# Optimization experiments

Measured on AMD Instinct MI355X. Metric: run time of the kernel, lower is better.

## Reference

```python
import jax, jax.numpy as jnp
import numpy as np

N = 80000
E = 1280000
IN_DIM = 512
OUT_DIM = 64
POS_DIM = 8
NEG_SLOPE = 0.01  # F.leaky_relu default


def setup_inputs() -> dict:
    key = jax.random.key(0)
    k1, k2, k3, k4, k5, k6 = jax.random.split(key, 6)
    h = jax.random.normal(k1, (N, IN_DIM), dtype=jnp.float32)
    pos = jax.random.normal(k2, (N, POS_DIM), dtype=jnp.float32)
    src = jax.random.randint(k3, (E,), 0, N, dtype=jnp.int32)
    dst = jax.random.randint(k4, (E,), 0, N, dtype=jnp.int32)
    W_fc = jax.random.normal(k5, (OUT_DIM, IN_DIM), dtype=jnp.float32) * (1.0 / np.sqrt(IN_DIM))
    W_attn = jax.random.normal(k6, (1, 2 * OUT_DIM + 2 * POS_DIM), dtype=jnp.float32) * 0.1
    return {"h": h, "pos": pos, "src": src, "dst": dst, "W_fc": W_fc, "W_attn": W_attn}


def reference(h, pos, src, dst, W_fc, W_attn):
    # node projection: z = fc(h)  [N, out]
    z = h @ W_fc.T
    # attn_fc applied to concat([z_src, z_dst, pos_src, pos_dst]) == split dot products
    wa = W_attn[0]
    w_zs = wa[:OUT_DIM]
    w_zd = wa[OUT_DIM:2 * OUT_DIM]
    w_ps = wa[2 * OUT_DIM:2 * OUT_DIM + POS_DIM]
    w_pd = wa[2 * OUT_DIM + POS_DIM:]
    el = z @ w_zs + pos @ w_ps  # [N] src-side score
    er = z @ w_zd + pos @ w_pd  # [N] dst-side score
    e = el[src] + er[dst]       # [E]
    e = jnp.where(e > 0, e, NEG_SLOPE * e)  # leaky_relu
    # segment softmax over incoming edges of each dst node (numerically stable)
    emax = jax.ops.segment_max(e, dst, num_segments=N)  # [N]
    ex = jnp.exp(e - emax[dst])                         # [E]
    denom = jax.ops.segment_sum(ex, dst, num_segments=N)  # [N]
    alpha = ex / denom[dst]                             # [E]
    # weighted scatter-sum of src features
    msgs = alpha[:, None] * z[src]                      # [E, out]
    h_out = jax.ops.segment_sum(msgs, dst, num_segments=N)  # [N, out]
    return h_out
```

## Files before the change

kernel.cpp:

```cpp
#include <hip/hip_runtime.h>
#include <math.h>

#define N_NODES 80000
#define E_EDGES 1280000
#define IN_DIM  512
#define OUT_DIM 64
#define POS_DIM 8
#define NEG_SLOPE 0.01f

#define NB_BUCKET 313
#define BCAP 8192
#define SCAT_CHUNK 4096
#define SCAT_NB 313
#define GEMM_NB 625

#define BM 128
#define BK 64
#define LDA 72
#define LDB 72

typedef __attribute__((ext_vector_type(8))) short short8v;
typedef __attribute__((ext_vector_type(4))) float f32x4;

__device__ __forceinline__ unsigned short f2bf(float f) {
    unsigned u = __float_as_uint(f);
    unsigned r = u + 0x7fff + ((u >> 16) & 1);
    return (unsigned short)(r >> 16);
}
__device__ __forceinline__ float lrelu(float e) { return e > 0.f ? e : NEG_SLOPE * e; }

__global__ __launch_bounds__(256) void gemm_scatter(const float* __restrict__ h,
                                                    const float* __restrict__ W,
                                                    const float* __restrict__ pos,
                                                    const float* __restrict__ Wa,
                                                    const int* __restrict__ src,
                                                    const int* __restrict__ dst,
                                                    char* __restrict__ zq,
                                                    float* __restrict__ scl,
                                                    float* __restrict__ el,
                                                    float* __restrict__ er,
                                                    int* __restrict__ bcnt,
                                                    int* __restrict__ ebuf) {
    __shared__ unsigned short sA[BM][LDA];
    __shared__ unsigned short sB[64][LDB];
    __shared__ int hh[NB_BUCKET];
    __shared__ int gb[NB_BUCKET];
    const int t = threadIdx.x;

    if (blockIdx.x >= GEMM_NB) {
        const int e0 = (blockIdx.x - GEMM_NB) * SCAT_CHUNK;
        for (int i = t; i < NB_BUCKET; i += 256) hh[i] = 0;
        __syncthreads();

        int key[16];
        short bk[16];
        short lr[16];
        #pragma unroll
        for (int r = 0; r < 16; ++r) {
            const int e = e0 + r * 256 + t;
            if (e < E_EDGES) {
                const int d = dst[e];
                const int s = src[e];
                bk[r]  = (short)(d >> 8);
                key[r] = (s << 8) | (d & 255);
                lr[r]  = (short)atomicAdd(&hh[d >> 8], 1);
            } else {
                bk[r] = -1;
            }
        }
        __syncthreads();

        for (int i = t; i < NB_BUCKET; i += 256) {
            const int c = hh[i];
            gb[i] = c ? (i * BCAP + atomicAdd(&bcnt[i], c)) : 0;
        }
        __syncthreads();

        #pragma unroll
        for (int r = 0; r < 16; ++r) {
            if (bk[r] >= 0) {
                ebuf[gb[bk[r]] + lr[r]] = key[r];
            }
        }
        return;
    }

    const int lane = t & 63;
    const int w    = t >> 6;
    const int row0 = blockIdx.x * BM;
    const int g    = lane >> 4;
    const int rr   = lane & 15;

    f32x4 acc[2][4] = {};
    float4 ra[8];
    float4 rb[4];

    {
        #pragma unroll
        for (int i = 0; i < 8; ++i) {
            const int idx = t + i * 256;
            ra[i] = *(const float4*)&h[(size_t)(row0 + (idx >> 4)) * IN_DIM + ((idx & 15) << 2)];
        }
        #pragma unroll
        for (int i = 0; i < 4; ++i) {
            const int idx = t + i * 256;
            rb[i] = *(const float4*)&W[(size_t)(idx >> 4) * IN_DIM + ((idx & 15) << 2)];
        }
    }

    for (int c = 0; c < IN_DIM / BK; ++c) {
        __syncthreads();
        #pragma unroll
        for (int i = 0; i < 8; ++i) {
            const int idx = t + i * 256;
            ushort4 v = {f2bf(ra[i].x), f2bf(ra[i].y), f2bf(ra[i].z), f2bf(ra[i].w)};
            *(ushort4*)&sA[idx >> 4][(idx & 15) << 2] = v;
        }
        #pragma unroll
        for (int i = 0; i < 4; ++i) {
            const int idx = t + i * 256;
            ushort4 v = {f2bf(rb[i].x), f2bf(rb[i].y), f2bf(rb[i].z), f2bf(rb[i].w)};
            *(ushort4*)&sB[idx >> 4][(idx & 15) << 2] = v;
        }
        __syncthreads();

        if (c < IN_DIM / BK - 1) {
            const int k0 = (c + 1) * BK;
            #pragma unroll
            for (int i = 0; i < 8; ++i) {
                const int idx = t + i * 256;
                ra[i] = *(const float4*)&h[(size_t)(row0 + (idx >> 4)) * IN_DIM + k0 + ((idx & 15) << 2)];
            }
            #pragma unroll
            for (int i = 0; i < 4; ++i) {
                const int idx = t + i * 256;
                rb[i] = *(const float4*)&W[(size_t)(idx >> 4) * IN_DIM + k0 + ((idx & 15) << 2)];
            }
        }

        short8v afr[2][2];
        #pragma unroll
        for (int rt = 0; rt < 2; ++rt)
            #pragma unroll
            for (int ks = 0; ks < 2; ++ks)
                afr[rt][ks] = *(const short8v*)&sA[w * 32 + rt * 16 + rr][ks * 32 + g * 8];
        short8v bfr[4][2];
        #pragma unroll
        for (int ct = 0; ct < 4; ++ct)
            #pragma unroll
            for (int ks = 0; ks < 2; ++ks)
                bfr[ct][ks] = *(const short8v*)&sB[ct * 16 + rr][ks * 32 + g * 8];

        #pragma unroll
        for (int ks = 0; ks < 2; ++ks)
            #pragma unroll
            for (int rt = 0; rt < 2; ++rt)
                #pragma unroll
                for (int ct = 0; ct < 4; ++ct)
                    acc[rt][ct] = __builtin_amdgcn_mfma_f32_16x16x32_bf16(
                        afr[rt][ks], bfr[ct][ks], acc[rt][ct], 0, 0, 0);
    }

    __syncthreads();
    char* sI8 = (char*)sB;

    float wzs_c[4], wzd_c[4];
    #pragma unroll
    for (int ct = 0; ct < 4; ++ct) {
        wzs_c[ct] = Wa[ct * 16 + rr];
        wzd_c[ct] = Wa[OUT_DIM + ct * 16 + rr];
    }
    #pragma unroll
    for (int rt = 0; rt < 2; ++rt)
        #pragma unroll
        for (int r = 0; r < 4; ++r) {
            float pe = 0.f, pd = 0.f, rmax = 0.f;
            #pragma unroll
            for (int ct = 0; ct < 4; ++ct) {
                const float v = acc[rt][ct][r];
                pe += v * wzs_c[ct];
                pd += v * wzd_c[ct];
                rmax = fmaxf(rmax, fabsf(v));
            }
            #pragma unroll
            for (int off = 8; off; off >>= 1) {
                pe += __shfl_xor(pe, off);
                pd += __shfl_xor(pd, off);
                rmax = fmaxf(rmax, __shfl_xor(rmax, off));
            }
            rmax = fmaxf(rmax, 1e-20f);
            const float inv_s = 127.f / rmax;
            const int rloc = w * 32 + rt * 16 + g * 4 + r;
            #pragma unroll
            for (int ct = 0; ct < 4; ++ct) {
                int q = __float2int_rn(acc[rt][ct][r] * inv_s);
                q = max(-127, min(127, q));
                sI8[rloc * 64 + ct * 16 + rr] = (char)q;
            }
            if (rr == 0) {
                const int row = row0 + rloc;
                scl[row] = rmax * (1.f / 127.f);
                const float4 p0 = *(const float4*)&pos[(size_t)row * POS_DIM];
                const float4 p1 = *(const float4*)&pos[(size_t)row * POS_DIM + 4];
                const float4 s0 = *(const float4*)&Wa[2 * OUT_DIM];
                const float4 s1 = *(const float4*)&Wa[2 * OUT_DIM + 4];
                const float4 d0 = *(const float4*)&Wa[2 * OUT_DIM + POS_DIM];
                const float4 d1 = *(const float4*)&Wa[2 * OUT_DIM + POS_DIM + 4];
                el[row] = pe + p0.x * s0.x + p0.y * s0.y + p0.z * s0.z + p0.w * s0.w
                              + p1.x * s1.x + p1.y * s1.y + p1.z * s1.z + p1.w * s1.w;
                er[row] = pd + p0.x * d0.x + p0.y * d0.y + p0.z * d0.z + p0.w * d0.w
                              + p1.x * d1.x + p1.y * d1.y + p1.z * d1.z + p1.w * d1.w;
            }
        }

    __syncthreads();
    uint4* g4 = (uint4*)(zq + (size_t)row0 * 64);
    const uint4* s4 = (const uint4*)sI8;
    g4[t] = s4[t];
    g4[t + 256] = s4[t + 256];
}

__global__ __launch_bounds__(256) void bucket_csr(int* __restrict__ ebuf,
                                                  const int* __restrict__ bcnt,
                                                  int* __restrict__ offs,
                                                  int* __restrict__ oend) {
    __shared__ int se[BCAP];
    __shared__ int cnt[256];
    __shared__ int cur[256];
    __shared__ int wt[4];
    const int b = blockIdx.x;
    const int t = threadIdx.x;
    const int lane = t & 63;
    const int w = t >> 6;
    const int lo = b * BCAP;
    const int ne = min(bcnt[b], BCAP);

    cnt[t] = 0;
    __syncthreads();

    for (int i = t; i < ne; i += 256) {
        const int k = ebuf[lo + i];
        atomicAdd(&cnt[k & 255], 1);
        se[i] = k;
    }
    __syncthreads();

    const int v = cnt[t];
    int s = v;
    #pragma unroll
    for (int off = 1; off < 64; off <<= 1) {
        const int u = __shfl_up(s, off);
        if (lane >= off) s += u;
    }
    if (lane == 63) wt[w] = s;
    __syncthreads();
    int base = 0;
    #pragma unroll
    for (int i = 0; i < 4; ++i)
        if (i < w) base += wt[i];
    const int excl = base + s - v;
    cur[t] = excl;
    const int node = b * 256 + t;
    if (node < N_NODES) {
        offs[node] = lo + excl;
        oend[node] = lo + excl + v;
    }
    __syncthreads();

    for (int i = t; i < ne; i += 256) {
        const int k = se[i];
        const int p = atomicAdd(&cur[k & 255], 1);
        ebuf[lo + p] = k >> 8;
    }
}

__global__ __launch_bounds__(256) void aggregate(const int* __restrict__ offs,
                                                 const int* __restrict__ oend,
                                                 const int* __restrict__ esrc,
                                                 const float* __restrict__ el,
                                                 const float* __restrict__ er,
                                                 const float* __restrict__ scl,
                                                 const char* __restrict__ zq,
                                                 float* __restrict__ out) {
    const int widx = (int)((blockIdx.x * 256 + threadIdx.x) >> 6);
    const int lane = threadIdx.x & 63;
    const int g = lane >> 4;
    const int u = lane & 15;
    const int d = widx * 4 + g;
    if (d >= N_NODES) return;
    const int start = offs[d];
    const int ne    = oend[d] - start;
    const float erd = er[d];
    const int bl = g << 4;

    int sA = 0, sB = 0;
    float eA = -INFINITY, eB = -INFINITY;
    if (u < ne) {
        sA = esrc[start + u];
        eA = lrelu(el[sA] + erd);
    }
    if (u + 16 < ne) {
        sB = esrc[start + u + 16];
        eB = lrelu(el[sB] + erd);
    }
    float m = fmaxf(eA, eB);
    for (int i = u + 32; i < ne; i += 16)
        m = fmaxf(m, lrelu(el[esrc[start + i]] + erd));
    #pragma unroll
    for (int off = 8; off; off >>= 1) m = fmaxf(m, __shfl_xor(m, off));

    const float exA = (u < ne) ? __expf(eA - m) : 0.f;
    const float exB = (u + 16 < ne) ? __expf(eB - m) : 0.f;
    float dsum = exA + exB;
    for (int i = u + 32; i < ne; i += 16)
        dsum += __expf(lrelu(el[esrc[start + i]] + erd) - m);
    #pragma unroll
    for (int off = 8; off; off >>= 1) dsum += __shfl_xor(dsum, off);

    float a0 = 0.f, a1 = 0.f, a2 = 0.f, a3 = 0.f;
    const int nreg = min(ne, 32);
    int bb = 0;
    for (; bb + 2 <= nreg; bb += 2) {
        const float w0 = (bb < 16)     ? __shfl(exA, bl + bb)      : __shfl(exB, bl + bb - 16);
        const int   s0 = (bb < 16)     ? __shfl(sA,  bl + bb)      : __shfl(sB,  bl + bb - 16);
        const float w1 = (bb + 1 < 16) ? __shfl(exA, bl + bb + 1)  : __shfl(exB, bl + bb - 15);
        const int   s1 = (bb + 1 < 16) ? __shfl(sA,  bl + bb + 1)  : __shfl(sB,  bl + bb - 15);
        const char4 z0 = *(const char4*)&zq[((size_t)s0 << 6) + (u << 2)];
        const char4 z1 = *(const char4*)&zq[((size_t)s1 << 6) + (u << 2)];
        const float wq0 = w0 * scl[s0];
        const float wq1 = w1 * scl[s1];
        a0 += wq0 * (float)z0.x; a1 += wq0 * (float)z0.y;
        a2 += wq0 * (float)z0.z; a3 += wq0 * (float)z0.w;
        a0 += wq1 * (float)z1.x; a1 += wq1 * (float)z1.y;
        a2 += wq1 * (float)z1.z; a3 += wq1 * (float)z1.w;
    }
    if (bb < nreg) {
        const float w0 = (bb < 16) ? __shfl(exA, bl + bb) : __shfl(exB, bl + bb - 16);
        const int   s0 = (bb < 16) ? __shfl(sA,  bl + bb) : __shfl(sB,  bl + bb - 16);
        const char4 z0 = *(const char4*)&zq[((size_t)s0 << 6) + (u << 2)];
        const float wq0 = w0 * scl[s0];
        a0 += wq0 * (float)z0.x; a1 += wq0 * (float)z0.y;
        a2 += wq0 * (float)z0.z; a3 += wq0 * (float)z0.w;
    }
    for (int i = 32; i < ne; ++i) {
        const int s = esrc[start + i];
        const float w0 = __expf(lrelu(el[s] + erd) - m);
        const char4 z0 = *(const char4*)&zq[((size_t)s << 6) + (u << 2)];
        const float wq0 = w0 * scl[s];
        a0 += wq0 * (float)z0.x; a1 += wq0 * (float)z0.y;
        a2 += wq0 * (float)z0.z; a3 += wq0 * (float)z0.w;
    }

    const float inv = (ne > 0) ? (1.f / dsum) : 0.f;
    float4 o = {a0 * inv, a1 * inv, a2 * inv, a3 * inv};
    *(float4*)&out[((size_t)d << 6) + (u << 2)] = o;
}

extern "C" void kernel_launch(void* const* d_in, const int* in_sizes, int n_in,
                              void* d_out, int out_size, void* d_ws, size_t ws_size,
                              hipStream_t stream) {
    const float* h   = (const float*)d_in[0];
    const float* pos = (const float*)d_in[1];
    const int* src   = (const int*)d_in[2];
    const int* dst   = (const int*)d_in[3];
    const float* Wfc = (const float*)d_in[4];
    const float* Wa  = (const float*)d_in[5];
    float* out = (float*)d_out;

    char* ws = (char*)d_ws;
    char*  zq   = (char*) (ws);
    float* scl  = (float*)(ws + 5120000);
    float* el   = (float*)(ws + 5440000);
    float* er   = (float*)(ws + 5760000);
    int*   offs = (int*)  (ws + 6080000);
    int*   oend = (int*)  (ws + 6400000);
    int*   ebuf = (int*)  (ws + 6720000);
    int*   bcnt = (int*)  (ws + 16976384);

    hipMemsetAsync(bcnt, 0, NB_BUCKET * sizeof(int), stream);
    gemm_scatter<<<GEMM_NB + SCAT_NB, 256, 0, stream>>>(h, Wfc, pos, Wa, src, dst,
                                                        zq, scl, el, er, bcnt, ebuf);
    bucket_csr<<<NB_BUCKET, 256, 0, stream>>>(ebuf, bcnt, offs, oend);
    aggregate<<<(N_NODES + 15) / 16, 256, 0, stream>>>(offs, oend, ebuf, el, er, scl, zq, out);
}
```

Measured before the change: 94.59 us.

## Fuse bucket CSR build into aggregation with smaller 64-node buckets

Buckets now cover 64 destination nodes (1250 buckets, capacity 2048) instead of 256. The CSR sort and the softmax aggregation run in one kernel, with the per-bucket sorted source list kept in shared memory, so the offs/oend arrays and the rewritten ebuf never go back to global memory. The scatter phase also reads src/dst with int4 vector loads. The trade-offs are fewer blocks in the aggregation (1250 blocks of 256 threads, each doing 4 node rounds per group), a bucket capacity that leaves less headroom against overflow (about 1024 edges expected per bucket), and more shared memory per block.

```diff
diff --git a/kernel.cpp b/kernel.cpp
--- a/kernel.cpp
+++ b/kernel.cpp
@@ -8,8 +8,8 @@
 #define POS_DIM 8
 #define NEG_SLOPE 0.01f
 
-#define NB_BUCKET 313
-#define BCAP 8192
+#define NB_BUCKET 1250
+#define BCAP 2048
 #define SCAT_CHUNK 4096
 #define SCAT_NB 313
 #define GEMM_NB 625
@@ -56,16 +56,32 @@
         short bk[16];
         short lr[16];
         #pragma unroll
-        for (int r = 0; r < 16; ++r) {
-            const int e = e0 + r * 256 + t;
-            if (e < E_EDGES) {
-                const int d = dst[e];
-                const int s = src[e];
-                bk[r]  = (short)(d >> 8);
-                key[r] = (s << 8) | (d & 255);
-                lr[r]  = (short)atomicAdd(&hh[d >> 8], 1);
+        for (int r4 = 0; r4 < 4; ++r4) {
+            const int e = e0 + r4 * 1024 + (t << 2);
+            if (e + 3 < E_EDGES) {
+                const int4 s4 = *(const int4*)&src[e];
+                const int4 d4 = *(const int4*)&dst[e];
+                bk[r4 * 4 + 0] = (short)(d4.x >> 6); key[r4 * 4 + 0] = (s4.x << 6) | (d4.x & 63);
+                lr[r4 * 4 + 0] = (short)atomicAdd(&hh[d4.x >> 6], 1);
+                bk[r4 * 4 + 1] = (short)(d4.y >> 6); key[r4 * 4 + 1] = (s4.y << 6) | (d4.y & 63);
+                lr[r4 * 4 + 1] = (short)atomicAdd(&hh[d4.y >> 6], 1);
+                bk[r4 * 4 + 2] = (short)(d4.z >> 6); key[r4 * 4 + 2] = (s4.z << 6) | (d4.z & 63);
+                lr[r4 * 4 + 2] = (short)atomicAdd(&hh[d4.z >> 6], 1);
+                bk[r4 * 4 + 3] = (short)(d4.w >> 6); key[r4 * 4 + 3] = (s4.w << 6) | (d4.w & 63);
+                lr[r4 * 4 + 3] = (short)atomicAdd(&hh[d4.w >> 6], 1);
             } else {
-                bk[r] = -1;
+                #pragma unroll
+                for (int j = 0; j < 4; ++j) {
+                    const int ee = e + j;
+                    if (ee < E_EDGES) {
+                        const int d = dst[ee];
+                        bk[r4 * 4 + j] = (short)(d >> 6);
+                        key[r4 * 4 + j] = (src[ee] << 6) | (d & 63);
+                        lr[r4 * 4 + j] = (short)atomicAdd(&hh[d >> 6], 1);
+                    } else {
+                        bk[r4 * 4 + j] = -1;
+                    }
+                }
             }
         }
         __syncthreads();
@@ -220,14 +236,18 @@
     g4[t + 256] = s4[t + 256];
 }
 
-__global__ __launch_bounds__(256) void bucket_csr(int* __restrict__ ebuf,
-                                                  const int* __restrict__ bcnt,
-                                                  int* __restrict__ offs,
-                                                  int* __restrict__ oend) {
+__global__ __launch_bounds__(256) void csr_aggregate(const int* __restrict__ ebuf,
+                                                     const int* __restrict__ bcnt,
+                                                     const float* __restrict__ el,
+                                                     const float* __restrict__ er,
+                                                     const float* __restrict__ scl,
+                                                     const char* __restrict__ zq,
+                                                     float* __restrict__ out) {
     __shared__ int se[BCAP];
-    __shared__ int cnt[256];
-    __shared__ int cur[256];
-    __shared__ int wt[4];
+    __shared__ int ss[BCAP];
+    __shared__ int cnt[64];
+    __shared__ int off0[64];
+    __shared__ int cur[64];
     const int b = blockIdx.x;
     const int t = threadIdx.x;
     const int lane = t & 63;
@@ -235,125 +255,111 @@
     const int lo = b * BCAP;
     const int ne = min(bcnt[b], BCAP);
 
-    cnt[t] = 0;
-    __syncthreads();
-
-    for (int i = t; i < ne; i += 256) {
-        const int k = ebuf[lo + i];
-        atomicAdd(&cnt[k & 255], 1);
-        se[i] = k;
-    }
-    __syncthreads();
-
-    const int v = cnt[t];
-    int s = v;
-    #pragma unroll
-    for (int off = 1; off < 64; off <<= 1) {
-        const int u = __shfl_up(s, off);
-        if (lane >= off) s += u;
-    }
-    if (lane == 63) wt[w] = s;
-    __syncthreads();
-    int base = 0;
-    #pragma unroll
-    for (int i = 0; i < 4; ++i)
-        if (i < w) base += wt[i];
-    const int excl = base + s - v;
-    cur[t] = excl;
-    const int node = b * 256 + t;
-    if (node < N_NODES) {
-        offs[node] = lo + excl;
-        oend[node] = lo + excl + v;
-    }
-    __syncthreads();
-
-    for (int i = t; i < ne; i += 256) {
-        const int k = se[i];
-        const int p = atomicAdd(&cur[k & 255], 1);
-        ebuf[lo + p] = k >> 8;
-    }
-}
-
-__global__ __launch_bounds__(256) void aggregate(const int* __restrict__ offs,
-                                                 const int* __restrict__ oend,
-                                                 const int* __restrict__ esrc,
-                                                 const float* __restrict__ el,
-                                                 const float* __restrict__ er,
-                                                 const float* __restrict__ scl,
-                                                 const char* __restrict__ zq,
-                                                 float* __restrict__ out) {
-    const int widx = (int)((blockIdx.x * 256 + threadIdx.x) >> 6);
-    const int lane = threadIdx.x & 63;
+    if (t < 64) cnt[t] = 0;
+    __syncthreads();
+
+    for (int i4 = t << 2; i4 < ne; i4 += 1024) {
+        const int4 k4 = *(const int4*)&ebuf[lo + i4];
+        if (i4 + 0 < ne) { se[i4 + 0] = k4.x; atomicAdd(&cnt[k4.x & 63], 1); }
+        if (i4 + 1 < ne) { se[i4 + 1] = k4.y; atomicAdd(&cnt[k4.y & 63], 1); }
+        if (i4 + 2 < ne) { se[i4 + 2] = k4.z; atomicAdd(&cnt[k4.z & 63], 1); }
+        if (i4 + 3 < ne) { se[i4 + 3] = k4.w; atomicAdd(&cnt[k4.w & 63], 1); }
+    }
+    __syncthreads();
+
+    if (t < 64) {
+        const int v = cnt[t];
+        int s = v;
+        #pragma unroll
+        for (int off = 1; off < 64; off <<= 1) {
+            const int u = __shfl_up(s, off);
+            if (lane >= off) s += u;
+        }
+        off0[t] = s - v;
+        cur[t]  = s - v;
+    }
+    __syncthreads();
+
+    for (int i4 = t << 2; i4 < ne; i4 += 1024) {
+        #pragma unroll
+        for (int j = 0; j < 4; ++j) {
+            if (i4 + j < ne) {
+                const int k = se[i4 + j];
+                const int p = atomicAdd(&cur[k & 63], 1);
+                ss[p] = k >> 6;
+            }
+        }
+    }
+    __syncthreads();
+
     const int g = lane >> 4;
     const int u = lane & 15;
-    const int d = widx * 4 + g;
-    if (d >= N_NODES) return;
-    const int start = offs[d];
-    const int ne    = oend[d] - start;
-    const float erd = er[d];
     const int bl = g << 4;
-
-    int sA = 0, sB = 0;
-    float eA = -INFINITY, eB = -INFINITY;
-    if (u < ne) {
-        sA = esrc[start + u];
-        eA = lrelu(el[sA] + erd);
-    }
-    if (u + 16 < ne) {
-        sB = esrc[start + u + 16];
-        eB = lrelu(el[sB] + erd);
-    }
-    float m = fmaxf(eA, eB);
-    for (int i = u + 32; i < ne; i += 16)
-        m = fmaxf(m, lrelu(el[esrc[start + i]] + erd));
-    #pragma unroll
-    for (int off = 8; off; off >>= 1) m = fmaxf(m, __shfl_xor(m, off));
-
-    const float exA = (u < ne) ? __expf(eA - m) : 0.f;
-    const float exB = (u + 16 < ne) ? __expf(eB - m) : 0.f;
-    float dsum = exA + exB;
-    for (int i = u + 32; i < ne; i += 16)
-        dsum += __expf(lrelu(el[esrc[start + i]] + erd) - m);
-    #pragma unroll
-    for (int off = 8; off; off >>= 1) dsum += __shfl_xor(dsum, off);
-
-    float a0 = 0.f, a1 = 0.f, a2 = 0.f, a3 = 0.f;
-    const int nreg = min(ne, 32);
-    int bb = 0;
-    for (; bb + 2 <= nreg; bb += 2) {
-        const float w0 = (bb < 16)     ? __shfl(exA, bl + bb)      : __shfl(exB, bl + bb - 16);
-        const int   s0 = (bb < 16)     ? __shfl(sA,  bl + bb)      : __shfl(sB,  bl + bb - 16);
-        const float w1 = (bb + 1 < 16) ? __shfl(exA, bl + bb + 1)  : __shfl(exB, bl + bb - 15);
-        const int   s1 = (bb + 1 < 16) ? __shfl(sA,  bl + bb + 1)  : __shfl(sB,  bl + bb - 15);
-        const char4 z0 = *(const char4*)&zq[((size_t)s0 << 6) + (u << 2)];
-        const char4 z1 = *(const char4*)&zq[((size_t)s1 << 6) + (u << 2)];
-        const float wq0 = w0 * scl[s0];
-        const float wq1 = w1 * scl[s1];
-        a0 += wq0 * (float)z0.x; a1 += wq0 * (float)z0.y;
-        a2 += wq0 * (float)z0.z; a3 += wq0 * (float)z0.w;
-        a0 += wq1 * (float)z1.x; a1 += wq1 * (float)z1.y;
-        a2 += wq1 * (float)z1.z; a3 += wq1 * (float)z1.w;
-    }
-    if (bb < nreg) {
-        const float w0 = (bb < 16) ? __shfl(exA, bl + bb) : __shfl(exB, bl + bb - 16);
-        const int   s0 = (bb < 16) ? __shfl(sA,  bl + bb) : __shfl(sB,  bl + bb - 16);
-        const char4 z0 = *(const char4*)&zq[((size_t)s0 << 6) + (u << 2)];
-        const float wq0 = w0 * scl[s0];
-        a0 += wq0 * (float)z0.x; a1 += wq0 * (float)z0.y;
-        a2 += wq0 * (float)z0.z; a3 += wq0 * (float)z0.w;
-    }
-    for (int i = 32; i < ne; ++i) {
-        const int s = esrc[start + i];
-        const float w0 = __expf(lrelu(el[s] + erd) - m);
-        const char4 z0 = *(const char4*)&zq[((size_t)s << 6) + (u << 2)];
-        const float wq0 = w0 * scl[s];
-        a0 += wq0 * (float)z0.x; a1 += wq0 * (float)z0.y;
-        a2 += wq0 * (float)z0.z; a3 += wq0 * (float)z0.w;
-    }
-
-    const float inv = (ne > 0) ? (1.f / dsum) : 0.f;
-    float4 o = {a0 * inv, a1 * inv, a2 * inv, a3 * inv};
-    *(float4*)&out[((size_t)d << 6) + (u << 2)] = o;
+    for (int r = 0; r < 4; ++r) {
+        const int dl = (w << 4) + (r << 2) + g;
+        const int d = (b << 6) + dl;
+        const int off = off0[dl];
+        const int nn = cnt[dl];
+        const float erd = er[d];
+
+        int sAi = 0, sBi = 0;
+        float eA = -INFINITY, eB = -INFINITY;
+        if (u < nn) {
+            sAi = ss[off + u];
+            eA = lrelu(el[sAi] + erd);
+        }
+        if (u + 16 < nn) {
+            sBi = ss[off + u + 16];
+            eB = lrelu(el[sBi] + erd);
+        }
+        float m = fmaxf(eA, eB);
+        for (int i = u + 32; i < nn; i += 16)
+            m = fmaxf(m, lrelu(el[ss[off + i]] + erd));
+        #pragma unroll
+        for (int off2 = 8; off2; off2 >>= 1) m = fmaxf(m, __shfl_xor(m, off2));
+
+        const float exA = (u < nn) ? __expf(eA - m) : 0.f;
+        const float exB = (u + 16 < nn) ? __expf(eB - m) : 0.f;
+        float dsum = exA + exB;
+        for (int i = u + 32; i < nn; i += 16)
+            dsum += __expf(lrelu(el[ss[off + i]] + erd) - m);
+        #pragma unroll
+        for (int off2 = 8; off2; off2 >>= 1) dsum += __shfl_xor(dsum, off2);
+
+        float a0 = 0.f, a1 = 0.f, a2 = 0.f, a3 = 0.f;
+        const int nreg = min(nn, 32);
+        for (int bb = 0; bb < nreg; bb += 4) {
+            float wj[4];
+            int sj[4];
+            #pragma unroll
+            for (int j = 0; j < 4; ++j) {
+                const int idx = bb + j;
+                wj[j] = (idx < 16) ? __shfl(exA, bl + idx) : __shfl(exB, bl + idx - 16);
+                sj[j] = (idx < 16) ? __shfl(sAi, bl + idx) : __shfl(sBi, bl + idx - 16);
+            }
+            #pragma unroll
+            for (int j = 0; j < 4; ++j) {
+                if (bb + j < nreg) {
+                    const char4 z = *(const char4*)&zq[((size_t)sj[j] << 6) + (u << 2)];
+                    const float wq = wj[j] * scl[sj[j]];
+                    a0 += wq * (float)z.x; a1 += wq * (float)z.y;
+                    a2 += wq * (float)z.z; a3 += wq * (float)z.w;
+                }
+            }
+        }
+        for (int i = 32; i < nn; ++i) {
+            const int s = ss[off + i];
+            const float w0 = __expf(lrelu(el[s] + erd) - m);
+            const char4 z = *(const char4*)&zq[((size_t)s << 6) + (u << 2)];
+            const float wq = w0 * scl[s];
+            a0 += wq * (float)z.x; a1 += wq * (float)z.y;
+            a2 += wq * (float)z.z; a3 += wq * (float)z.w;
+        }
+
+        const float inv = (nn > 0) ? (1.f / dsum) : 0.f;
+        float4 o = {a0 * inv, a1 * inv, a2 * inv, a3 * inv};
+        *(float4*)&out[((size_t)d << 6) + (u << 2)] = o;
+    }
 }
 
 extern "C" void kernel_launch(void* const* d_in, const int* in_sizes, int n_in,
@@ -372,14 +378,11 @@
     float* scl  = (float*)(ws + 5120000);
     float* el   = (float*)(ws + 5440000);
     float* er   = (float*)(ws + 5760000);
-    int*   offs = (int*)  (ws + 6080000);
-    int*   oend = (int*)  (ws + 6400000);
-    int*   ebuf = (int*)  (ws + 6720000);
-    int*   bcnt = (int*)  (ws + 16976384);
+    int*   ebuf = (int*)  (ws + 6080000);
+    int*   bcnt = (int*)  (ws + 16320000);
 
     hipMemsetAsync(bcnt, 0, NB_BUCKET * sizeof(int), stream);
     gemm_scatter<<<GEMM_NB + SCAT_NB, 256, 0, stream>>>(h, Wfc, pos, Wa, src, dst,
                                                         zq, scl, el, er, bcnt, ebuf);
-    bucket_csr<<<NB_BUCKET, 256, 0, stream>>>(ebuf, bcnt, offs, oend);
-    aggregate<<<(N_NODES + 15) / 16, 256, 0, stream>>>(offs, oend, ebuf, el, er, scl, zq, out);
+    csr_aggregate<<<NB_BUCKET, 256, 0, stream>>>(ebuf, bcnt, el, er, scl, zq, out);
 }
```

Result: faster. 92.51 us (-2.2%).
